# Optimization experiments

Measured on AMD Instinct MI355X. Metric: run time of the kernel, lower is better.

## Reference

```python
import jax, jax.numpy as jnp
import numpy as np

E = 262144   # number of half-edges / feature rows
C = 128      # in_channels
K = 4        # neighbors per half-edge
O = 256      # out_channels


def setup_inputs() -> dict:
    key = jax.random.key(0)
    k1, k2, k3, k4 = jax.random.split(key, 4)
    x = jax.random.normal(k1, (E, C), dtype=jnp.float32)
    neighbor_idx = jax.random.randint(k2, (E, K), 0, E, dtype=jnp.int64)
    W = jax.random.normal(k3, (K * C, O), dtype=jnp.float32) / np.sqrt(K * C)
    b = jax.random.normal(k4, (O,), dtype=jnp.float32) * 0.01
    return {"x": x, "neighbor_idx": neighbor_idx, "W": W, "b": b}


def reference(x, neighbor_idx, W, b):
    # gather neighbor features: [E, K, C] -> concat -> [E, K*C]
    gathered = x[neighbor_idx].reshape(x.shape[0], -1)
    # Linear + ReLU, batched over all half-edges
    out = jnp.maximum(gathered @ W + b, 0.0)
    return out
```

## Files before the change

### kernel.cpp

```cpp
#include <hip/hip_runtime.h>
#include <hip/hip_bf16.h>


#define E_ROWS 262144
#define C_IN   128
#define KN     4
#define O_OUT  256
#define BM     128
#define BN     128
#define BK     32
#define NSTEPS 16
#define NT     512

typedef __attribute__((ext_vector_type(8))) short bf16x8;
typedef __attribute__((ext_vector_type(4))) float f32x4;

__device__ __forceinline__ unsigned short bf16_rne(float f) {
    unsigned u = __float_as_uint(f);
    return (unsigned short)((u + 0x7fffu + ((u >> 16) & 1u)) >> 16);
}

__global__ void prep_w(const float* __restrict__ W, uint4* __restrict__ wimg) {
    __shared__ float Ws[32][260];
    const int s = blockIdx.x;
    const int t = threadIdx.x;
    #pragma unroll
    for (int i = 0; i < 8; ++i) {
        int v4 = i * 256 + t;
        int k  = v4 >> 6;
        int n4 = v4 & 63;
        float4 w = ((const float4*)W)[(size_t)(s * 32 + k) * 64 + n4];
        *(float4*)&Ws[k][n4 * 4] = w;
    }
    __syncthreads();
    #pragma unroll
    for (int i = 0; i < 8; ++i) {
        int q  = i * 256 + t;
        int nb = q >> 10;
        int h  = (q >> 9) & 1;
        int cl = q & 511;
        int nl = cl >> 2;
        int cs = cl & 3;
        int c  = cs ^ ((nl >> 1) & 3);
        int n  = nb * 128 + nl;
        int kb = c * 8;
        unsigned short v[8];
        #pragma unroll
        for (int e = 0; e < 8; ++e) {
            float w = Ws[kb + e][n];
            unsigned u  = __float_as_uint(w);
            unsigned hb = (u + 0x7fffu + ((u >> 16) & 1u)) & 0xffff0000u;
            float r = w - __uint_as_float(hb);
            v[e] = h ? bf16_rne(r) : (unsigned short)(hb >> 16);
        }
        uint4 o;
        o.x = (unsigned)v[0] | ((unsigned)v[1] << 16);
        o.y = (unsigned)v[2] | ((unsigned)v[3] << 16);
        o.z = (unsigned)v[4] | ((unsigned)v[5] << 16);
        o.w = (unsigned)v[6] | ((unsigned)v[7] << 16);
        wimg[(size_t)nb * 16384 + (size_t)(2 * s + h) * 512 + cl] = o;
    }
}

__global__ __launch_bounds__(NT, 4) void gemm(
    const float* __restrict__ x,
    const int* __restrict__ nidx,
    const uint4* __restrict__ wimg,
    const float* __restrict__ bias,
    float* __restrict__ out)
{
    __shared__ __align__(16) float A_s[2][BM * BK];
    __shared__ __align__(16) unsigned short B_s[2][2 * BN * BK];
    __shared__ int   idx_s[BM * KN];
    __shared__ float b_s[BN];

    const int t  = threadIdx.x;
    const int m0 = blockIdx.x * BM;
    const int nb = blockIdx.y;
    const int n0 = nb * BN;

    idx_s[t] = nidx[(size_t)m0 * KN + t];
    if (t < BN) b_s[t] = bias[n0 + t];

    const int l   = t & 63;
    const int wid = t >> 6;
    const int wm  = wid >> 1;
    const int wn  = wid & 1;
    const int lr  = l & 15;
    const int lg  = l >> 4;

    const int arow0 = t >> 3;
    const int ac0   = (t & 7) ^ (arow0 & 7);
    const int arow1 = (512 + t) >> 3;
    const int ac1   = ((512 + t) & 7) ^ (arow1 & 7);

    const uint4* wbase = wimg + (size_t)nb * 16384;

    f32x4 acc[2][4];
    #pragma unroll
    for (int i = 0; i < 2; ++i)
        #pragma unroll
        for (int jj = 0; jj < 4; ++jj)
            acc[i][jj] = (f32x4){0.f, 0.f, 0.f, 0.f};

    char* Aall = (char*)&A_s[0][0];
    char* Ball = (char*)&B_s[0][0];

    auto STAGE = [&](int s, int buf) {
        const int j  = s >> 2;
        const int kc = (s & 3) << 5;
        char* Ab = Aall + (buf << 14);
        char* Bb = Ball + (buf << 14);
        const float* a0p = x + (size_t)idx_s[arow0 * KN + j] * C_IN + kc + (ac0 << 2);
        const float* a1p = x + (size_t)idx_s[arow1 * KN + j] * C_IN + kc + (ac1 << 2);
        __builtin_amdgcn_global_load_lds(
            (const __attribute__((address_space(1))) void*)a0p,
            (__attribute__((address_space(3))) void*)(Ab + (wid << 10)), 16, 0, 0);
        __builtin_amdgcn_global_load_lds(
            (const __attribute__((address_space(1))) void*)a1p,
            (__attribute__((address_space(3))) void*)(Ab + 8192 + (wid << 10)), 16, 0, 0);
        const uint4* sH = wbase + (size_t)(2 * s) * 512 + t;
        const uint4* sL = wbase + (size_t)(2 * s + 1) * 512 + t;
        __builtin_amdgcn_global_load_lds(
            (const __attribute__((address_space(1))) void*)sH,
            (__attribute__((address_space(3))) void*)(Bb + (wid << 10)), 16, 0, 0);
        __builtin_amdgcn_global_load_lds(
            (const __attribute__((address_space(1))) void*)sL,
            (__attribute__((address_space(3))) void*)(Bb + 8192 + (wid << 10)), 16, 0, 0);
    };

    auto COMPUTE = [&](int buf) {
        char* Ab = Aall + (buf << 14);
        char* Bb = Ball + (buf << 14);
        bf16x8 bh[4], bl[4];
        #pragma unroll
        for (int nf = 0; nf < 4; ++nf) {
            int nl  = (wn << 6) + (nf << 4) + lr;
            int cB  = lg ^ ((nl >> 1) & 3);
            int off = nl * 64 + cB * 16;
            bh[nf] = *(const bf16x8*)(Bb + off);
            bl[nf] = *(const bf16x8*)(Bb + 8192 + off);
        }
        #pragma unroll
        for (int mf = 0; mf < 2; ++mf) {
            int row = (wm << 5) + (mf << 4) + lr;
            int c0  = (lg << 1) ^ (row & 7);
            f32x4 a0 = *(const f32x4*)(Ab + row * 128 + c0 * 16);
            f32x4 a1 = *(const f32x4*)(Ab + row * 128 + (c0 ^ 1) * 16);
            float av[8];
            av[0]=a0[0]; av[1]=a0[1]; av[2]=a0[2]; av[3]=a0[3];
            av[4]=a1[0]; av[5]=a1[1]; av[6]=a1[2]; av[7]=a1[3];
            bf16x8 ah, al;
            #pragma unroll
            for (int e = 0; e < 8; ++e) {
                unsigned u  = __float_as_uint(av[e]);
                unsigned hb = u & 0xffff0000u;
                ah[e] = (short)(u >> 16);
                al[e] = (short)bf16_rne(av[e] - __uint_as_float(hb));
            }
            #pragma unroll
            for (int nf = 0; nf < 4; ++nf) {
                acc[mf][nf] = __builtin_amdgcn_mfma_f32_16x16x32_bf16(ah, bh[nf], acc[mf][nf], 0, 0, 0);
                acc[mf][nf] = __builtin_amdgcn_mfma_f32_16x16x32_bf16(ah, bl[nf], acc[mf][nf], 0, 0, 0);
                acc[mf][nf] = __builtin_amdgcn_mfma_f32_16x16x32_bf16(al, bh[nf], acc[mf][nf], 0, 0, 0);
            }
        }
    };

    __syncthreads();
    STAGE(0, 0);
    __syncthreads();

    #pragma unroll 1
    for (int s = 0; s < NSTEPS; s += 2) {
        if (s + 1 < NSTEPS) STAGE(s + 1, 1);
        COMPUTE(0);
        __syncthreads();
        if (s + 2 < NSTEPS) STAGE(s + 2, 0);
        COMPUTE(1);
        __syncthreads();
    }

    #pragma unroll
    for (int mf = 0; mf < 2; ++mf) {
        #pragma unroll
        for (int nf = 0; nf < 4; ++nf) {
            int colL = (wn << 6) + (nf << 4) + lr;
            int col  = n0 + colL;
            float bv = b_s[colL];
            int rowb = m0 + (wm << 5) + (mf << 4) + (lg << 2);
            #pragma unroll
            for (int r = 0; r < 4; ++r) {
                float v = acc[mf][nf][r] + bv;
                out[(size_t)(rowb + r) * O_OUT + col] = fmaxf(v, 0.f);
            }
        }
    }
}

extern "C" void kernel_launch(void* const* d_in, const int* in_sizes, int n_in,
                              void* d_out, int out_size, void* d_ws, size_t ws_size,
                              hipStream_t stream) {
    const float* x    = (const float*)d_in[0];
    const int*   nidx = (const int*)d_in[1];
    const float* W    = (const float*)d_in[2];
    const float* bias = (const float*)d_in[3];
    float* out  = (float*)d_out;
    uint4* wimg = (uint4*)d_ws;

    hipLaunchKernelGGL(prep_w, dim3(NSTEPS), dim3(256), 0, stream, W, wimg);
    hipLaunchKernelGGL(gemm, dim3(E_ROWS / BM, O_OUT / BN), dim3(NT), 0, stream,
                       x, nidx, wimg, bias, out);
}
```

Measured before the change: 543.1 us.

## Stage gather loads through registers and swizzle block order for L2 reuse

Replaces the direct global-to-LDS async loads with a register-staged, two-deep prefetch pipeline: loads for stage s+2 are issued into registers while stage s is computed, then written to LDS before the next barrier. Neighbor indices now sit in per-thread registers instead of a shared index table. A 1D block-ID remap places the two N-halves of each M tile, in groups of 8 M tiles, next to each other in launch order, so the gathered x rows are more likely to be reused from L2. The register staging raises VGPR pressure and adds explicit LDS writes, which may hurt occupancy.

New measurement: 611.0 us. 12.5% more time.

```diff
diff --git a/kernel.cpp b/kernel.cpp
--- a/kernel.cpp
+++ b/kernel.cpp
@@ -62,6 +62,34 @@
     }
 }
 
+#define ISSUE(S, SL) do {                                                   \
+    int j_  = (S) >> 2;                                                     \
+    int kc_ = ((S) & 3) << 5;                                               \
+    int i0_ = (j_ & 2) ? ((j_ & 1) ? ib0_3 : ib0_2)                         \
+                       : ((j_ & 1) ? ib0_1 : ib0_0);                        \
+    int i1_ = (j_ & 2) ? ((j_ & 1) ? ib1_3 : ib1_2)                         \
+                       : ((j_ & 1) ? ib1_1 : ib1_0);                        \
+    rA0_##SL = *(const uint4*)(x + (size_t)i0_ * C_IN + kc_ + (ac0 << 2));  \
+    rA1_##SL = *(const uint4*)(x + (size_t)i1_ * C_IN + kc_ + (ac0 << 2));  \
+    const uint4* wp_ = wbase + (size_t)(2 * (S)) * 512 + t;                 \
+    rBH_##SL = wp_[0];                                                      \
+    rBL_##SL = wp_[512];                                                    \
+} while (0)
+
+#define WRITEB(SL, PW) do {                                                 \
+    char* Ab_ = Aall + ((PW) << 14);                                        \
+    char* Bb_ = Ball + ((PW) << 14);                                        \
+    *(uint4*)(Ab_ + t * 16)        = rA0_##SL;                              \
+    *(uint4*)(Ab_ + 8192 + t * 16) = rA1_##SL;                              \
+    *(uint4*)(Bb_ + t * 16)        = rBH_##SL;                              \
+    *(uint4*)(Bb_ + 8192 + t * 16) = rBL_##SL;                              \
+} while (0)
+
+#define BARRIER() do {                                                      \
+    asm volatile("s_waitcnt lgkmcnt(0)" ::: "memory");                      \
+    __builtin_amdgcn_s_barrier();                                           \
+} while (0)
+
 __global__ __launch_bounds__(NT, 4) void gemm(
     const float* __restrict__ x,
     const int* __restrict__ nidx,
@@ -71,15 +99,16 @@
 {
     __shared__ __align__(16) float A_s[2][BM * BK];
     __shared__ __align__(16) unsigned short B_s[2][2 * BN * BK];
-    __shared__ int   idx_s[BM * KN];
     __shared__ float b_s[BN];
 
-    const int t  = threadIdx.x;
-    const int m0 = blockIdx.x * BM;
-    const int nb = blockIdx.y;
-    const int n0 = nb * BN;
-
-    idx_s[t] = nidx[(size_t)m0 * KN + t];
+    const int t = threadIdx.x;
+
+    const int L    = blockIdx.x + blockIdx.y * 2048;
+    const int mblk = (L & 7) | ((L >> 4) << 3);
+    const int nb   = (L >> 3) & 1;
+    const int m0   = mblk * BM;
+    const int n0   = nb * BN;
+
     if (t < BN) b_s[t] = bias[n0 + t];
 
     const int l   = t & 63;
@@ -91,8 +120,15 @@
 
     const int arow0 = t >> 3;
     const int ac0   = (t & 7) ^ (arow0 & 7);
-    const int arow1 = (512 + t) >> 3;
-    const int ac1   = ((512 + t) & 7) ^ (arow1 & 7);
+
+    const int ib0_0 = nidx[(size_t)(m0 + arow0) * KN + 0];
+    const int ib0_1 = nidx[(size_t)(m0 + arow0) * KN + 1];
+    const int ib0_2 = nidx[(size_t)(m0 + arow0) * KN + 2];
+    const int ib0_3 = nidx[(size_t)(m0 + arow0) * KN + 3];
+    const int ib1_0 = nidx[(size_t)(m0 + 64 + arow0) * KN + 0];
+    const int ib1_1 = nidx[(size_t)(m0 + 64 + arow0) * KN + 1];
+    const int ib1_2 = nidx[(size_t)(m0 + 64 + arow0) * KN + 2];
+    const int ib1_3 = nidx[(size_t)(m0 + 64 + arow0) * KN + 3];
 
     const uint4* wbase = wimg + (size_t)nb * 16384;
 
@@ -106,32 +142,12 @@
     char* Aall = (char*)&A_s[0][0];
     char* Ball = (char*)&B_s[0][0];
 
-    auto STAGE = [&](int s, int buf) {
-        const int j  = s >> 2;
-        const int kc = (s & 3) << 5;
-        char* Ab = Aall + (buf << 14);
-        char* Bb = Ball + (buf << 14);
-        const float* a0p = x + (size_t)idx_s[arow0 * KN + j] * C_IN + kc + (ac0 << 2);
-        const float* a1p = x + (size_t)idx_s[arow1 * KN + j] * C_IN + kc + (ac1 << 2);
-        __builtin_amdgcn_global_load_lds(
-            (const __attribute__((address_space(1))) void*)a0p,
-            (__attribute__((address_space(3))) void*)(Ab + (wid << 10)), 16, 0, 0);
-        __builtin_amdgcn_global_load_lds(
-            (const __attribute__((address_space(1))) void*)a1p,
-            (__attribute__((address_space(3))) void*)(Ab + 8192 + (wid << 10)), 16, 0, 0);
-        const uint4* sH = wbase + (size_t)(2 * s) * 512 + t;
-        const uint4* sL = wbase + (size_t)(2 * s + 1) * 512 + t;
-        __builtin_amdgcn_global_load_lds(
-            (const __attribute__((address_space(1))) void*)sH,
-            (__attribute__((address_space(3))) void*)(Bb + (wid << 10)), 16, 0, 0);
-        __builtin_amdgcn_global_load_lds(
-            (const __attribute__((address_space(1))) void*)sL,
-            (__attribute__((address_space(3))) void*)(Bb + 8192 + (wid << 10)), 16, 0, 0);
-    };
-
-    auto COMPUTE = [&](int buf) {
-        char* Ab = Aall + (buf << 14);
-        char* Bb = Ball + (buf << 14);
+    uint4 rA0_0, rA1_0, rBH_0, rBL_0;
+    uint4 rA0_1, rA1_1, rBH_1, rBL_1;
+
+    auto COMPUTE = [&](int p) {
+        char* Ab = Aall + (p << 14);
+        char* Bb = Ball + (p << 14);
         bf16x8 bh[4], bl[4];
         #pragma unroll
         for (int nf = 0; nf < 4; ++nf) {
@@ -167,19 +183,27 @@
         }
     };
 
-    __syncthreads();
-    STAGE(0, 0);
-    __syncthreads();
+    ISSUE(0, 0);
+    ISSUE(1, 1);
+    WRITEB(0, 0);
+    ISSUE(2, 0);
+    BARRIER();
 
     #pragma unroll 1
-    for (int s = 0; s < NSTEPS; s += 2) {
-        if (s + 1 < NSTEPS) STAGE(s + 1, 1);
+    for (int s = 0; s < 12; s += 2) {
+        WRITEB(1, 1);
+        ISSUE(s + 3, 1);
         COMPUTE(0);
-        __syncthreads();
-        if (s + 2 < NSTEPS) STAGE(s + 2, 0);
+        BARRIER();
+        WRITEB(0, 0);
+        ISSUE(s + 4, 0);
         COMPUTE(1);
-        __syncthreads();
-    }
+        BARRIER();
+    }
+    WRITEB(1, 1); ISSUE(15, 1); COMPUTE(0); BARRIER();
+    WRITEB(0, 0);               COMPUTE(1); BARRIER();
+    WRITEB(1, 1);               COMPUTE(0); BARRIER();
+    COMPUTE(1);
 
     #pragma unroll
     for (int mf = 0; mf < 2; ++mf) {
@@ -209,6 +233,6 @@
     uint4* wimg = (uint4*)d_ws;
 
     hipLaunchKernelGGL(prep_w, dim3(NSTEPS), dim3(256), 0, stream, W, wimg);
-    hipLaunchKernelGGL(gemm, dim3(E_ROWS / BM, O_OUT / BN), dim3(NT), 0, stream,
+    hipLaunchKernelGGL(gemm, dim3(2048, 2), dim3(NT), 0, stream,
                        x, nidx, wimg, bias, out);
 }
```
